# Performance work log

Measured on AMD Instinct MI355X. Metric: run time of the kernel, lower is better.

## Reference

```python
import jax, jax.numpy as jnp
import numpy as np

N, T, D = 64, 2048, 512
NEG = -1e9


def setup_inputs() -> dict:
    key = jax.random.key(0)
    k1, k2, k3, k4 = jax.random.split(key, 4)
    return {
        "query": jax.random.normal(k1, (N, D), dtype=jnp.float32),
        "key": jax.random.normal(k2, (T, N, D), dtype=jnp.float32),
        "value": jax.random.normal(k3, (T, N, D), dtype=jnp.float32),
        "lens": jax.random.randint(k4, (N,), 0, T, dtype=jnp.int64)
        if jax.config.jax_enable_x64 else jax.random.randint(k4, (N,), 0, T, dtype=jnp.int32),
    }


def reference(query, key, value, lens):
    # key/value: (T, N, D) -> (N, T, D)
    k = jnp.transpose(key, (1, 0, 2))
    v = jnp.transpose(value, (1, 0, 2))
    # energy: (N, T) = per-batch matvec key @ query
    energy = jnp.einsum('ntd,nd->nt', k, query)
    # length mask: positions >= lens are masked with -1e9 (as in masked_fill_)
    mask = jnp.arange(energy.shape[1])[None, :] >= lens[:, None]
    energy = jnp.where(mask, jnp.asarray(NEG, energy.dtype), energy)
    attention = jax.nn.softmax(energy, axis=1)
    # context: (N, D)
    context = jnp.einsum('nt,ntd->nd', attention, v)
    return context
```

## Files before the change

kernel.cpp:

```cpp
#include <hip/hip_runtime.h>
#include <math.h>

#define N_B 64
#define T_LEN 2048
#define D_DIM 512
#define NEG (-1e9f)
#define G_BLK 2048
#define MIN_W 16
#define J_MAX 132


__device__ __forceinline__ float dot8(const float4& qa, const float4& qb,
                                      const float4& ka, const float4& kb) {
    return qa.x * ka.x + qa.y * ka.y + qa.z * ka.z + qa.w * ka.w
         + qb.x * kb.x + qb.y * kb.y + qb.z * kb.z + qb.w * kb.w;
}

__device__ __forceinline__ int useful_rows(int len) {
    return (len == 0) ? T_LEN : len;
}

__global__ __launch_bounds__(256) void attn_partial(
    const float* __restrict__ q,
    const float* __restrict__ key,
    const float* __restrict__ val,
    const int*   __restrict__ lens,
    float* __restrict__ m_ws,
    float* __restrict__ l_ws,
    float* __restrict__ o_ws)
{
    const int tid  = threadIdx.x;
    const int wave = tid >> 6;
    const int lane = tid & 63;
    const int d0   = 2 * tid;
    const size_t rstride = (size_t)N_B * D_DIM;

    __shared__ int   pre_sm[N_B + 1];
    __shared__ float acc_sm[4][D_DIM];
    __shared__ float ml_sm[4][2];

    if (wave == 0) {
        int incl = useful_rows(lens[lane]);
        #pragma unroll
        for (int off = 1; off < 64; off <<= 1) {
            const int y = __shfl_up(incl, off);
            if (lane >= off) incl += y;
        }
        if (lane == 0) pre_sm[0] = 0;
        pre_sm[1 + lane] = incl;
    }
    __syncthreads();

    const int total = pre_sm[N_B];
    int W = (total + G_BLK - 1) / G_BLK;
    if (W < MIN_W) W = MIN_W;
    const int r0 = blockIdx.x * W;
    if (r0 >= total) return;
    const int r1 = min(r0 + W, total);

    int lo = 0, hi = N_B;
    while (hi - lo > 1) {
        const int mid = (lo + hi) >> 1;
        if (pre_sm[mid] <= r0) lo = mid; else hi = mid;
    }
    int n = lo;
    int r = r0;

    while (r < r1) {
        const int sn    = pre_sm[n];
        const int sn1   = pre_sm[n + 1];
        const int ta    = r - sn;
        const int tb    = min(r1, sn1) - sn;
        const int j     = blockIdx.x - (sn / W);
        const int len_n = lens[n];

        float acc[8];
        #pragma unroll
        for (int jj = 0; jj < 8; ++jj) acc[jj] = 0.0f;
        float m = -INFINITY, l = 0.0f;

        if (len_n == 0) {
            int cnt = 0;
            const float* vr = val + ((size_t)(ta + wave) * N_B + n) * D_DIM
                            + 8 * lane;
            for (int t = ta + wave; t < tb; t += 4) {
                const float4 va = *reinterpret_cast<const float4*>(vr);
                const float4 vb = *reinterpret_cast<const float4*>(vr + 4);
                vr += 4 * rstride;
                acc[0] += va.x; acc[1] += va.y; acc[2] += va.z; acc[3] += va.w;
                acc[4] += vb.x; acc[5] += vb.y; acc[6] += vb.z; acc[7] += vb.w;
                ++cnt;
            }
            m = NEG;
            l = (float)cnt;
        } else {
            int t = ta + wave;
            if (t < tb) {
                const float4* q4 = reinterpret_cast<const float4*>(
                    q + (size_t)n * D_DIM) + 2 * lane;
                const float4 qa = q4[0];
                const float4 qb = q4[1];

                const float* kr = key + ((size_t)t * N_B + n) * D_DIM + 8 * lane;
                const float* vr = val + ((size_t)t * N_B + n) * D_DIM + 8 * lane;

                float4 ka = *reinterpret_cast<const float4*>(kr);
                float4 kb = *reinterpret_cast<const float4*>(kr + 4);
                float4 na = ka, nb = kb;

                for (; t < tb; t += 4) {
                    const float4 va = *reinterpret_cast<const float4*>(vr);
                    const float4 vb = *reinterpret_cast<const float4*>(vr + 4);
                    vr += 4 * rstride;
                    if (t + 4 < tb) {
                        na = *reinterpret_cast<const float4*>(kr + 4 * rstride);
                        nb = *reinterpret_cast<const float4*>(kr + 4 * rstride + 4);
                    }
                    kr += 4 * rstride;

                    float e = dot8(qa, qb, ka, kb);
                    #pragma unroll
                    for (int off = 32; off; off >>= 1) e += __shfl_xor(e, off);

                    if (e > m) {
                        const float sc = __expf(m - e);
                        l *= sc;
                        #pragma unroll
                        for (int jj = 0; jj < 8; ++jj) acc[jj] *= sc;
                        m = e;
                    }
                    const float p = __expf(e - m);
                    l += p;
                    acc[0] += p * va.x; acc[1] += p * va.y;
                    acc[2] += p * va.z; acc[3] += p * va.w;
                    acc[4] += p * vb.x; acc[5] += p * vb.y;
                    acc[6] += p * vb.z; acc[7] += p * vb.w;

                    ka = na; kb = nb;
                }
            }
        }

        *reinterpret_cast<float4*>(&acc_sm[wave][8 * lane]) =
            make_float4(acc[0], acc[1], acc[2], acc[3]);
        *reinterpret_cast<float4*>(&acc_sm[wave][8 * lane + 4]) =
            make_float4(acc[4], acc[5], acc[6], acc[7]);
        if (lane == 0) { ml_sm[wave][0] = m; ml_sm[wave][1] = l; }
        __syncthreads();

        const float m0 = ml_sm[0][0], m1 = ml_sm[1][0];
        const float m2 = ml_sm[2][0], m3 = ml_sm[3][0];
        const float M  = fmaxf(fmaxf(m0, m1), fmaxf(m2, m3));
        const float s0 = __expf(m0 - M), s1 = __expf(m1 - M);
        const float s2 = __expf(m2 - M), s3 = __expf(m3 - M);

        float2 rr;
        rr.x = s0 * acc_sm[0][d0]     + s1 * acc_sm[1][d0]
             + s2 * acc_sm[2][d0]     + s3 * acc_sm[3][d0];
        rr.y = s0 * acc_sm[0][d0 + 1] + s1 * acc_sm[1][d0 + 1]
             + s2 * acc_sm[2][d0 + 1] + s3 * acc_sm[3][d0 + 1];
        *reinterpret_cast<float2*>(
            o_ws + ((size_t)n * J_MAX + j) * D_DIM + d0) = rr;

        if (tid == 0) {
            m_ws[n * J_MAX + j] = M;
            l_ws[n * J_MAX + j] = s0 * ml_sm[0][1] + s1 * ml_sm[1][1]
                                + s2 * ml_sm[2][1] + s3 * ml_sm[3][1];
        }

        r = min(r1, sn1);
        ++n;
        if (r < r1) __syncthreads();
    }
}

__global__ __launch_bounds__(256) void attn_combine(
    const int*   __restrict__ lens,
    const float* __restrict__ m_ws,
    const float* __restrict__ l_ws,
    const float* __restrict__ o_ws,
    float* __restrict__ out)
{
    const int n   = blockIdx.x;
    const int tid = threadIdx.x;

    __shared__ float s_sm[J_MAX];
    __shared__ float S_sm;
    __shared__ int   J_sm;

    if (tid < 64) {
        int incl = useful_rows(lens[tid]);
        #pragma unroll
        for (int off = 1; off < 64; off <<= 1) {
            const int y = __shfl_up(incl, off);
            if (tid >= off) incl += y;
        }
        const int total = __shfl(incl, 63);
        int W = (total + G_BLK - 1) / G_BLK;
        if (W < MIN_W) W = MIN_W;
        const int sn1 = __shfl(incl, n);
        const int sn  = (n == 0) ? 0 : __shfl(incl, n - 1);
        const int b0  = sn / W;
        const int b1  = (sn1 - 1) / W;
        const int J   = b1 - b0 + 1;
        if (tid == 0) J_sm = J;

        float mj[3], lj[3];
        float M = -INFINITY;
        #pragma unroll
        for (int k = 0; k < 3; ++k) {
            const int jdx = tid + 64 * k;
            const bool ok = (jdx < J);
            mj[k] = ok ? m_ws[n * J_MAX + jdx] : -INFINITY;
            lj[k] = ok ? l_ws[n * J_MAX + jdx] : 0.0f;
            M = fmaxf(M, mj[k]);
        }
        #pragma unroll
        for (int off = 32; off; off >>= 1) M = fmaxf(M, __shfl_xor(M, off));
        float S = 0.0f;
        #pragma unroll
        for (int k = 0; k < 3; ++k) {
            const int jdx = tid + 64 * k;
            const float s = __expf(mj[k] - M);
            if (jdx < J) s_sm[jdx] = s;
            S += s * lj[k];
        }
        #pragma unroll
        for (int off = 32; off; off >>= 1) S += __shfl_xor(S, off);
        if (tid == 0) S_sm = S;
    }
    __syncthreads();

    const int J = J_sm;
    const float inv = 1.0f / S_sm;
    const int d = blockIdx.y * 256 + tid;
    const float* op = o_ws + (size_t)n * J_MAX * D_DIM + d;

    float a0 = 0.0f, a1 = 0.0f, a2 = 0.0f, a3 = 0.0f;
    int jj = 0;
    for (; jj + 3 < J; jj += 4) {
        a0 += s_sm[jj]     * op[(size_t)jj * D_DIM];
        a1 += s_sm[jj + 1] * op[(size_t)(jj + 1) * D_DIM];
        a2 += s_sm[jj + 2] * op[(size_t)(jj + 2) * D_DIM];
        a3 += s_sm[jj + 3] * op[(size_t)(jj + 3) * D_DIM];
    }
    for (; jj < J; ++jj)
        a0 += s_sm[jj] * op[(size_t)jj * D_DIM];

    out[(size_t)n * D_DIM + d] = (a0 + a1 + a2 + a3) * inv;
}

extern "C" void kernel_launch(void* const* d_in, const int* in_sizes, int n_in,
                              void* d_out, int out_size, void* d_ws, size_t ws_size,
                              hipStream_t stream) {
    const float* q    = (const float*)d_in[0];
    const float* key  = (const float*)d_in[1];
    const float* val  = (const float*)d_in[2];
    const int*   lens = (const int*)d_in[3];
    float*       out  = (float*)d_out;

    float* m_ws = (float*)d_ws;
    float* l_ws = m_ws + N_B * J_MAX;
    float* o_ws = l_ws + N_B * J_MAX;

    attn_partial<<<G_BLK, 256, 0, stream>>>(q, key, val, lens,
                                            m_ws, l_ws, o_ws);
    attn_combine<<<dim3(N_B, D_DIM / 256), 256, 0, stream>>>(lens, m_ws, l_ws,
                                                             o_ws, out);
}
```

Before: 54.20 us.

## Use nontemporal K/V loads, shrink grid, add occupancy hint, unroll combine

Key and value streams now use nontemporal loads, so single-use data is less likely to pollute cache. The partial grid shrinks from 2048 to 1792 blocks, and launch bounds request 7 blocks per CU, which may limit registers. The combine kernel's reduction over partials is unrolled by 8 with tree summation to expose more memory-level parallelism. These are several independent tweaks to a bandwidth-bound streaming kernel.

```diff
diff --git a/kernel.cpp b/kernel.cpp
--- a/kernel.cpp
+++ b/kernel.cpp
@@ -5,13 +5,19 @@
 #define T_LEN 2048
 #define D_DIM 512
 #define NEG (-1e9f)
-#define G_BLK 2048
+#define G_BLK 1792
 #define MIN_W 16
 #define J_MAX 132
 
 
-__device__ __forceinline__ float dot8(const float4& qa, const float4& qb,
-                                      const float4& ka, const float4& kb) {
+typedef float fx4 __attribute__((ext_vector_type(4)));
+
+__device__ __forceinline__ fx4 ldnt4(const float* p) {
+    return __builtin_nontemporal_load(reinterpret_cast<const fx4*>(p));
+}
+
+__device__ __forceinline__ float dot8(const fx4& qa, const fx4& qb,
+                                      const fx4& ka, const fx4& kb) {
     return qa.x * ka.x + qa.y * ka.y + qa.z * ka.z + qa.w * ka.w
          + qb.x * kb.x + qb.y * kb.y + qb.z * kb.z + qb.w * kb.w;
 }
@@ -20,7 +26,7 @@
     return (len == 0) ? T_LEN : len;
 }
 
-__global__ __launch_bounds__(256) void attn_partial(
+__global__ __launch_bounds__(256, 7) void attn_partial(
     const float* __restrict__ q,
     const float* __restrict__ key,
     const float* __restrict__ val,
@@ -84,8 +90,8 @@
             const float* vr = val + ((size_t)(ta + wave) * N_B + n) * D_DIM
                             + 8 * lane;
             for (int t = ta + wave; t < tb; t += 4) {
-                const float4 va = *reinterpret_cast<const float4*>(vr);
-                const float4 vb = *reinterpret_cast<const float4*>(vr + 4);
+                const fx4 va = ldnt4(vr);
+                const fx4 vb = ldnt4(vr + 4);
                 vr += 4 * rstride;
                 acc[0] += va.x; acc[1] += va.y; acc[2] += va.z; acc[3] += va.w;
                 acc[4] += vb.x; acc[5] += vb.y; acc[6] += vb.z; acc[7] += vb.w;
@@ -96,25 +102,24 @@
         } else {
             int t = ta + wave;
             if (t < tb) {
-                const float4* q4 = reinterpret_cast<const float4*>(
-                    q + (size_t)n * D_DIM) + 2 * lane;
-                const float4 qa = q4[0];
-                const float4 qb = q4[1];
+                const float* qp = q + (size_t)n * D_DIM + 8 * lane;
+                const fx4 qa = *reinterpret_cast<const fx4*>(qp);
+                const fx4 qb = *reinterpret_cast<const fx4*>(qp + 4);
 
                 const float* kr = key + ((size_t)t * N_B + n) * D_DIM + 8 * lane;
                 const float* vr = val + ((size_t)t * N_B + n) * D_DIM + 8 * lane;
 
-                float4 ka = *reinterpret_cast<const float4*>(kr);
-                float4 kb = *reinterpret_cast<const float4*>(kr + 4);
-                float4 na = ka, nb = kb;
+                fx4 ka = ldnt4(kr);
+                fx4 kb = ldnt4(kr + 4);
+                fx4 na = ka, nb = kb;
 
                 for (; t < tb; t += 4) {
-                    const float4 va = *reinterpret_cast<const float4*>(vr);
-                    const float4 vb = *reinterpret_cast<const float4*>(vr + 4);
+                    const fx4 va = ldnt4(vr);
+                    const fx4 vb = ldnt4(vr + 4);
                     vr += 4 * rstride;
                     if (t + 4 < tb) {
-                        na = *reinterpret_cast<const float4*>(kr + 4 * rstride);
-                        nb = *reinterpret_cast<const float4*>(kr + 4 * rstride + 4);
+                        na = ldnt4(kr + 4 * rstride);
+                        nb = ldnt4(kr + 4 * rstride + 4);
                     }
                     kr += 4 * rstride;
 
@@ -236,18 +241,23 @@
     const int d = blockIdx.y * 256 + tid;
     const float* op = o_ws + (size_t)n * J_MAX * D_DIM + d;
 
-    float a0 = 0.0f, a1 = 0.0f, a2 = 0.0f, a3 = 0.0f;
+    float a0 = 0, a1 = 0, a2 = 0, a3 = 0, a4 = 0, a5 = 0, a6 = 0, a7 = 0;
     int jj = 0;
-    for (; jj + 3 < J; jj += 4) {
+    for (; jj + 7 < J; jj += 8) {
         a0 += s_sm[jj]     * op[(size_t)jj * D_DIM];
         a1 += s_sm[jj + 1] * op[(size_t)(jj + 1) * D_DIM];
         a2 += s_sm[jj + 2] * op[(size_t)(jj + 2) * D_DIM];
         a3 += s_sm[jj + 3] * op[(size_t)(jj + 3) * D_DIM];
+        a4 += s_sm[jj + 4] * op[(size_t)(jj + 4) * D_DIM];
+        a5 += s_sm[jj + 5] * op[(size_t)(jj + 5) * D_DIM];
+        a6 += s_sm[jj + 6] * op[(size_t)(jj + 6) * D_DIM];
+        a7 += s_sm[jj + 7] * op[(size_t)(jj + 7) * D_DIM];
     }
     for (; jj < J; ++jj)
         a0 += s_sm[jj] * op[(size_t)jj * D_DIM];
 
-    out[(size_t)n * D_DIM + d] = (a0 + a1 + a2 + a3) * inv;
+    out[(size_t)n * D_DIM + d] =
+        (((a0 + a1) + (a2 + a3)) + ((a4 + a5) + (a6 + a7))) * inv;
 }
 
 extern "C" void kernel_launch(void* const* d_in, const int* in_sizes, int n_in,
```

Measured after the change: 81.98 us. 1.51x slower.
